# Kernel tuning notes

Measured on AMD Instinct MI355X. Metric: run time of the kernel, lower is better.

Reference implementation:

```python
import jax, jax.numpy as jnp
import numpy as np

N_FRAMES = 64
N_ATOMS = 512
SEG_LEN = 1


def get_segments(n_atoms: int, length: int) -> np.ndarray:
    """All ordered pairs of chain segments (i,i+L),(j,j+L) that share no atoms (j-i>L)."""
    starts = np.arange(n_atoms - length)
    i, j = np.meshgrid(starts, starts, indexing='ij')
    mask = (j - i) > length
    i, j = i[mask], j[mask]
    return np.stack([i, i + length, j, j + length], axis=1).astype(np.int32)


def setup_inputs() -> dict:
    key = jax.random.key(0)
    xyz = jax.random.normal(key, (N_FRAMES, N_ATOMS, 3), dtype=jnp.float32)
    segments = jnp.asarray(get_segments(N_ATOMS, SEG_LEN))  # (P, 4) int32
    return {"xyz": xyz, "segments": segments}


def _unit(v):
    return v / jnp.linalg.norm(v, axis=-1, keepdims=True)


def reference(xyz, segments):
    # xyz: (F, N, 3); segments: (P, 4) = [i, i+L, j, j+L]
    p1 = xyz[:, segments[:, 0]]  # (F, P, 3)
    p2 = xyz[:, segments[:, 1]]
    p3 = xyz[:, segments[:, 2]]
    p4 = xyz[:, segments[:, 3]]

    r12 = p2 - p1
    r13 = p3 - p1
    r14 = p4 - p1
    r23 = p3 - p2
    r24 = p4 - p2
    r34 = p4 - p3

    # unit normals of the four faces of the tetrahedron spanned by the segment pair
    n1 = _unit(jnp.cross(r13, r14))
    n2 = _unit(jnp.cross(r14, r24))
    n3 = _unit(jnp.cross(r24, r23))
    n4 = _unit(jnp.cross(r23, r13))

    def asin_dot(a, b):
        return jnp.arcsin(jnp.clip(jnp.sum(a * b, axis=-1), -1.0, 1.0))

    # Gauss linking integral (Klenin & Langowski) per segment pair
    theta = asin_dot(n1, n2) + asin_dot(n2, n3) + asin_dot(n3, n4) + asin_dot(n4, n1)
    sign = jnp.sign(jnp.sum(jnp.cross(r34, r12) * r13, axis=-1))
    wr = theta * sign / (2.0 * jnp.pi)  # (F, P)
    return wr
```

## Files before the change

### kernel.cpp

```cpp
#include <hip/hip_runtime.h>
#include <math.h>

#define NFRAMES 64
#define NATOMS  512
#define NSEG    129795
#define NPAIR2  ((NSEG + 1) / 2)
#define BLOCK   256

typedef float v2 __attribute__((ext_vector_type(2)));

__device__ __forceinline__ v2 v2s(float x) { v2 r; r.x = x; r.y = x; return r; }
__device__ __forceinline__ v2 vfma(v2 a, v2 b, v2 c) { return __builtin_elementwise_fma(a, b, c); }

__device__ __forceinline__ v2 vabs(v2 x) {
    v2 r; r.x = fabsf(x.x); r.y = fabsf(x.y); return r;
}
__device__ __forceinline__ v2 vmin1(v2 a) {
    v2 r; r.x = fminf(a.x, 1.0f); r.y = fminf(a.y, 1.0f); return r;
}
__device__ __forceinline__ v2 vsqrt_raw(v2 x) {
    v2 r;
    r.x = __builtin_amdgcn_sqrtf(x.x);
    r.y = __builtin_amdgcn_sqrtf(x.y);
    return r;
}
__device__ __forceinline__ v2 vrsq_raw(v2 x) {
    v2 r;
    r.x = __builtin_amdgcn_rsqf(x.x);
    r.y = __builtin_amdgcn_rsqf(x.y);
    return r;
}
__device__ __forceinline__ v2 vcopysign(v2 m, v2 s) {
    v2 r; r.x = copysignf(m.x, s.x); r.y = copysignf(m.y, s.y); return r;
}

__device__ __forceinline__ v2 vasin(v2 x) {
    v2 ax = vmin1(vabs(x));
    v2 p  = vfma(ax, vfma(ax, vfma(ax, v2s(-0.0187293f), v2s(0.0742610f)), v2s(-0.2121144f)), v2s(1.5707288f));
    v2 r  = v2s(1.57079632679f) - vsqrt_raw(v2s(1.0f) - ax) * p;
    return vcopysign(r, x);
}

struct v23 { v2 x, y, z; };

__device__ __forceinline__ v23 vsub(v23 a, v23 b) { return v23{a.x - b.x, a.y - b.y, a.z - b.z}; }
__device__ __forceinline__ v23 vcross(v23 a, v23 b) {
    return v23{ vfma(a.y, b.z, -(a.z * b.y)),
                vfma(a.z, b.x, -(a.x * b.z)),
                vfma(a.x, b.y, -(a.y * b.x)) };
}
__device__ __forceinline__ v2 vdot(v23 a, v23 b) {
    return vfma(a.x, b.x, vfma(a.y, b.y, a.z * b.z));
}

__global__ __launch_bounds__(BLOCK) void writhe_kernel(
    const float* __restrict__ xyz,
    const int4*  __restrict__ segs,
    float*       __restrict__ out)
{
    __shared__ float4 sp[NATOMS];

    const int f = blockIdx.y;
    const float* fx = xyz + (size_t)f * (NATOMS * 3);
    for (int a = threadIdx.x; a < NATOMS; a += BLOCK) {
        const float* g = fx + 3 * a;
        sp[a] = make_float4(g[0], g[1], g[2], 0.0f);
    }
    __syncthreads();

    const int t  = blockIdx.x * BLOCK + threadIdx.x;
    const int s0 = 2 * t;
    if (s0 >= NSEG) return;
    const int s1 = (s0 + 1 < NSEG) ? (s0 + 1) : s0;

    const int4 g0 = segs[s0];
    const int4 g1 = segs[s1];

    float4 a1 = sp[g0.x], a2 = sp[g0.y], a3 = sp[g0.z], a4 = sp[g0.w];
    float4 b1 = sp[g1.x], b2 = sp[g1.y], b3 = sp[g1.z], b4 = sp[g1.w];

    v23 p1{{a1.x, b1.x}, {a1.y, b1.y}, {a1.z, b1.z}};
    v23 p2{{a2.x, b2.x}, {a2.y, b2.y}, {a2.z, b2.z}};
    v23 p3{{a3.x, b3.x}, {a3.y, b3.y}, {a3.z, b3.z}};
    v23 p4{{a4.x, b4.x}, {a4.y, b4.y}, {a4.z, b4.z}};

    v23 r12 = vsub(p2, p1);
    v23 r13 = vsub(p3, p1);
    v23 r14 = vsub(p4, p1);
    v23 r23 = vsub(p3, p2);
    v23 r24 = vsub(p4, p2);
    v23 r34 = vsub(p4, p3);

    v23 c1 = vcross(r13, r14);
    v23 c2 = vcross(r14, r24);
    v23 c3 = vcross(r24, r23);
    v23 c4 = vcross(r23, r13);

    v2 in1 = vrsq_raw(vdot(c1, c1));
    v2 in2 = vrsq_raw(vdot(c2, c2));
    v2 in3 = vrsq_raw(vdot(c3, c3));
    v2 in4 = vrsq_raw(vdot(c4, c4));

    v2 d12 = vdot(c1, c2) * (in1 * in2);
    v2 d23 = vdot(c2, c3) * (in2 * in3);
    v2 d34 = vdot(c3, c4) * (in3 * in4);
    v2 d41 = vdot(c4, c1) * (in4 * in1);

    v2 theta = (vasin(d12) + vasin(d23)) + (vasin(d34) + vasin(d41));

    v2 sv = vdot(vcross(r34, r12), r13);

    float w0 = theta.x * ((sv.x > 0.0f) ? 1.0f : ((sv.x < 0.0f) ? -1.0f : 0.0f)) * 0.15915494309189535f;
    float w1 = theta.y * ((sv.y > 0.0f) ? 1.0f : ((sv.y < 0.0f) ? -1.0f : 0.0f)) * 0.15915494309189535f;

    const size_t base = (size_t)f * NSEG;
    out[base + s0] = w0;
    if (s0 + 1 < NSEG) out[base + s0 + 1] = w1;
}

extern "C" void kernel_launch(void* const* d_in, const int* in_sizes, int n_in,
                              void* d_out, int out_size, void* d_ws, size_t ws_size,
                              hipStream_t stream) {
    const float* xyz  = (const float*)d_in[0];
    const int4*  segs = (const int4*)d_in[1];
    float*       out  = (float*)d_out;

    dim3 grid((NPAIR2 + BLOCK - 1) / BLOCK, NFRAMES);
    writhe_kernel<<<grid, BLOCK, 0, stream>>>(xyz, segs, out);
}
```

Baseline: 90.51 us.

## Derive segment pairs from row index instead of reading segment table

Each block now handles one row i of the pair triangle for one frame, and the j indices are computed directly rather than loaded from the segments array. Each thread handles four consecutive pairs and shares neighbouring atom loads from padded shared memory. This removes the global index traffic and reduces LDS reads. In exchange, the kernel depends on the fixed ordering of the segment list, and short rows leave many threads idle.

```diff
diff --git a/kernel.cpp b/kernel.cpp
--- a/kernel.cpp
+++ b/kernel.cpp
@@ -4,31 +4,21 @@
 #define NFRAMES 64
 #define NATOMS  512
 #define NSEG    129795
-#define NPAIR2  ((NSEG + 1) / 2)
-#define BLOCK   256
+#define NROWS   509
+#define BLOCK   128
+#define LDS_SLOTS 576
 
 typedef float v2 __attribute__((ext_vector_type(2)));
 
 __device__ __forceinline__ v2 v2s(float x) { v2 r; r.x = x; r.y = x; return r; }
 __device__ __forceinline__ v2 vfma(v2 a, v2 b, v2 c) { return __builtin_elementwise_fma(a, b, c); }
-
-__device__ __forceinline__ v2 vabs(v2 x) {
-    v2 r; r.x = fabsf(x.x); r.y = fabsf(x.y); return r;
-}
-__device__ __forceinline__ v2 vmin1(v2 a) {
-    v2 r; r.x = fminf(a.x, 1.0f); r.y = fminf(a.y, 1.0f); return r;
-}
+__device__ __forceinline__ v2 vabs(v2 x) { v2 r; r.x = fabsf(x.x); r.y = fabsf(x.y); return r; }
+__device__ __forceinline__ v2 vmin1(v2 a) { v2 r; r.x = fminf(a.x, 1.0f); r.y = fminf(a.y, 1.0f); return r; }
 __device__ __forceinline__ v2 vsqrt_raw(v2 x) {
-    v2 r;
-    r.x = __builtin_amdgcn_sqrtf(x.x);
-    r.y = __builtin_amdgcn_sqrtf(x.y);
-    return r;
+    v2 r; r.x = __builtin_amdgcn_sqrtf(x.x); r.y = __builtin_amdgcn_sqrtf(x.y); return r;
 }
 __device__ __forceinline__ v2 vrsq_raw(v2 x) {
-    v2 r;
-    r.x = __builtin_amdgcn_rsqf(x.x);
-    r.y = __builtin_amdgcn_rsqf(x.y);
-    return r;
+    v2 r; r.x = __builtin_amdgcn_rsqf(x.x); r.y = __builtin_amdgcn_rsqf(x.y); return r;
 }
 __device__ __forceinline__ v2 vcopysign(v2 m, v2 s) {
     v2 r; r.x = copysignf(m.x, s.x); r.y = copysignf(m.y, s.y); return r;
@@ -53,37 +43,7 @@
     return vfma(a.x, b.x, vfma(a.y, b.y, a.z * b.z));
 }
 
-__global__ __launch_bounds__(BLOCK) void writhe_kernel(
-    const float* __restrict__ xyz,
-    const int4*  __restrict__ segs,
-    float*       __restrict__ out)
-{
-    __shared__ float4 sp[NATOMS];
-
-    const int f = blockIdx.y;
-    const float* fx = xyz + (size_t)f * (NATOMS * 3);
-    for (int a = threadIdx.x; a < NATOMS; a += BLOCK) {
-        const float* g = fx + 3 * a;
-        sp[a] = make_float4(g[0], g[1], g[2], 0.0f);
-    }
-    __syncthreads();
-
-    const int t  = blockIdx.x * BLOCK + threadIdx.x;
-    const int s0 = 2 * t;
-    if (s0 >= NSEG) return;
-    const int s1 = (s0 + 1 < NSEG) ? (s0 + 1) : s0;
-
-    const int4 g0 = segs[s0];
-    const int4 g1 = segs[s1];
-
-    float4 a1 = sp[g0.x], a2 = sp[g0.y], a3 = sp[g0.z], a4 = sp[g0.w];
-    float4 b1 = sp[g1.x], b2 = sp[g1.y], b3 = sp[g1.z], b4 = sp[g1.w];
-
-    v23 p1{{a1.x, b1.x}, {a1.y, b1.y}, {a1.z, b1.z}};
-    v23 p2{{a2.x, b2.x}, {a2.y, b2.y}, {a2.z, b2.z}};
-    v23 p3{{a3.x, b3.x}, {a3.y, b3.y}, {a3.z, b3.z}};
-    v23 p4{{a4.x, b4.x}, {a4.y, b4.y}, {a4.z, b4.z}};
-
+__device__ __forceinline__ v2 writhe2(const v23& p1, const v23& p2, const v23& p3, const v23& p4) {
     v23 r12 = vsub(p2, p1);
     v23 r13 = vsub(p3, p1);
     v23 r14 = vsub(p4, p1);
@@ -109,22 +69,68 @@
     v2 theta = (vasin(d12) + vasin(d23)) + (vasin(d34) + vasin(d41));
 
     v2 sv = vdot(vcross(r34, r12), r13);
+    v2 sgn;
+    sgn.x = (sv.x > 0.0f) ? 1.0f : ((sv.x < 0.0f) ? -1.0f : 0.0f);
+    sgn.y = (sv.y > 0.0f) ? 1.0f : ((sv.y < 0.0f) ? -1.0f : 0.0f);
+    return theta * sgn * v2s(0.15915494309189535f);
+}
 
-    float w0 = theta.x * ((sv.x > 0.0f) ? 1.0f : ((sv.x < 0.0f) ? -1.0f : 0.0f)) * 0.15915494309189535f;
-    float w1 = theta.y * ((sv.y > 0.0f) ? 1.0f : ((sv.y < 0.0f) ? -1.0f : 0.0f)) * 0.15915494309189535f;
+__device__ __forceinline__ int slot_of(int a) { return a + (a >> 3); }
 
-    const size_t base = (size_t)f * NSEG;
-    out[base + s0] = w0;
-    if (s0 + 1 < NSEG) out[base + s0 + 1] = w1;
+__global__ __launch_bounds__(BLOCK) void writhe_kernel(
+    const float* __restrict__ xyz,
+    float*       __restrict__ out)
+{
+    __shared__ float4 sp[LDS_SLOTS];
+
+    const int i = blockIdx.x;
+    const int f = blockIdx.y;
+    const float* fx = xyz + (size_t)f * (NATOMS * 3);
+    for (int a = threadIdx.x; a < NATOMS; a += BLOCK) {
+        const float* g = fx + 3 * a;
+        sp[slot_of(a)] = make_float4(g[0], g[1], g[2], 0.0f);
+    }
+    __syncthreads();
+
+    const int len = NROWS - i;
+    const int t4  = threadIdx.x * 4;
+    if (t4 >= len) return;
+    const int jb  = i + 2 + t4;
+
+    float4 A0 = sp[slot_of(min(jb,     511))];
+    float4 A1 = sp[slot_of(min(jb + 1, 511))];
+    float4 A2 = sp[slot_of(min(jb + 2, 511))];
+    float4 A3 = sp[slot_of(min(jb + 3, 511))];
+    float4 A4 = sp[slot_of(min(jb + 4, 511))];
+
+    float4 P1 = sp[slot_of(i)];
+    float4 P2 = sp[slot_of(i + 1)];
+    v23 p1{v2s(P1.x), v2s(P1.y), v2s(P1.z)};
+    v23 p2{v2s(P2.x), v2s(P2.y), v2s(P2.z)};
+
+    v23 p3A{{A0.x, A1.x}, {A0.y, A1.y}, {A0.z, A1.z}};
+    v23 p4A{{A1.x, A2.x}, {A1.y, A2.y}, {A1.z, A2.z}};
+    v23 p3B{{A2.x, A3.x}, {A2.y, A3.y}, {A2.z, A3.z}};
+    v23 p4B{{A3.x, A4.x}, {A3.y, A4.y}, {A3.z, A4.z}};
+
+    v2 wA = writhe2(p1, p2, p3A, p4A);
+    v2 wB = writhe2(p1, p2, p3B, p4B);
+
+    const int off  = NROWS * i - (i * (i - 1)) / 2;
+    const size_t obase = (size_t)f * NSEG + off + t4;
+    const int rem = len - t4;
+    out[obase] = wA.x;
+    if (rem > 1) out[obase + 1] = wA.y;
+    if (rem > 2) out[obase + 2] = wB.x;
+    if (rem > 3) out[obase + 3] = wB.y;
 }
 
 extern "C" void kernel_launch(void* const* d_in, const int* in_sizes, int n_in,
                               void* d_out, int out_size, void* d_ws, size_t ws_size,
                               hipStream_t stream) {
-    const float* xyz  = (const float*)d_in[0];
-    const int4*  segs = (const int4*)d_in[1];
-    float*       out  = (float*)d_out;
+    const float* xyz = (const float*)d_in[0];
+    float*       out = (float*)d_out;
 
-    dim3 grid((NPAIR2 + BLOCK - 1) / BLOCK, NFRAMES);
-    writhe_kernel<<<grid, BLOCK, 0, stream>>>(xyz, segs, out);
+    dim3 grid(NROWS, NFRAMES);
+    writhe_kernel<<<grid, BLOCK, 0, stream>>>(xyz, out);
 }
```

After: 99.86 us. 1.1x slower.
